# Kernel tuning notes

Hardware: AMD Instinct MI355X
Metric: run time of the kernel (lower is better)

## Reference

```python
import jax, jax.numpy as jnp
import numpy as np

B, K, D, LS, NL = 32, 64, 256, 128, 2


def _xavier(key, shape):
    # torch xavier_uniform for Linear weight [out, in]
    fan_out, fan_in = shape[-2], shape[-1]
    lim = float(np.sqrt(6.0 / (fan_in + fan_out)))
    return jax.random.uniform(key, shape, jnp.float32, -lim, lim)


def setup_inputs():
    key = jax.random.key(0)
    ks = jax.random.split(key, 32)
    inp = {
        "X": jax.random.normal(ks[0], (B, K, D), jnp.float32),
        # per-layer stacked params [NL, ...]
        "k_w": _xavier(ks[1], (NL, D, D)),
        "q_w": _xavier(ks[2], (NL, D, D)),
        "rv_w1": _xavier(ks[3], (NL, D, 2 * D)),
        "rv_b1": jnp.zeros((NL, D), jnp.float32),
        "rv_w2": _xavier(ks[4], (NL, D, D)),
        "rv_b2": jnp.zeros((NL, D), jnp.float32),
        "ln_g": jnp.ones((NL, D), jnp.float32),
        "ln_b": jnp.zeros((NL, D), jnp.float32),
        "mlp_w1": _xavier(ks[5], (NL, D, D)),
        "mlp_b1": jnp.zeros((NL, D), jnp.float32),
        "mlp_w2": _xavier(ks[6], (NL, D, D)),
        "mlp_b2": jnp.zeros((NL, D), jnp.float32),
        "proj_w": _xavier(ks[7], (LS, D)),
        "proj_b": jnp.zeros((LS,), jnp.float32),
        "mu_w": _xavier(ks[8], (LS, LS)),
        "mu_b": jnp.zeros((LS,), jnp.float32),
        "sp_w": _xavier(ks[9], (LS, LS)),
        "sp_b": jnp.zeros((LS,), jnp.float32),
    }
    return inp


def _gelu(x):
    return jax.nn.gelu(x, approximate=False)


def _layernorm(x, g, b, eps=1e-5):
    m = jnp.mean(x, axis=-1, keepdims=True)
    v = jnp.mean((x - m) ** 2, axis=-1, keepdims=True)
    return (x - m) / jnp.sqrt(v + eps) * g + b


def _block(x, kw, qw, rw1, rb1, rw2, rb2, lg, lb, mw1, mb1, mw2, mb2):
    scale = D ** (-0.5)
    x_orig = x
    # pairwise difference r[b,i,j,:] = x[b,i]-x[b,j]
    r = x[:, :, None, :] - x[:, None, :, :]                      # [B,K,K,D]
    xi = jnp.broadcast_to(x[:, :, None, :], (B, K, K, D))
    cat = jnp.concatenate([xi, r], axis=-1)                      # [B,K,K,2D]
    v = _gelu(jnp.einsum('bijc,dc->bijd', cat, rw1) + rb1)
    v = jnp.einsum('bijd,ed->bije', v, rw2) + rb2                # [B,K,K,D]
    k = jnp.einsum('bid,ed->bie', x, kw)
    q = jnp.einsum('bid,ed->bie', x, qw) * scale
    attn = jax.nn.softmax(jnp.einsum('bid,bjd->bij', q, k), axis=2)
    agg = jnp.einsum('bij,bijd->bid', attn, v)
    h = _layernorm(x_orig + agg, lg, lb)
    h = jnp.einsum('bid,ed->bie', _gelu(jnp.einsum('bid,ed->bie', h, mw1) + mb1), mw2) + mb2
    return x_orig + h


def reference(X, k_w, q_w, rv_w1, rv_b1, rv_w2, rv_b2, ln_g, ln_b,
              mlp_w1, mlp_b1, mlp_w2, mlp_b2, proj_w, proj_b,
              mu_w, mu_b, sp_w, sp_b):
    x = X
    for i in range(NL):
        x = _block(x, k_w[i], q_w[i], rv_w1[i], rv_b1[i], rv_w2[i], rv_b2[i],
                   ln_g[i], ln_b[i], mlp_w1[i], mlp_b1[i], mlp_w2[i], mlp_b2[i])
    s = jnp.sum(x, axis=1)                                        # [B,D]
    h = _gelu(s @ proj_w.T + proj_b)                              # [B,LS]
    mu = h @ mu_w.T + mu_b
    scale = jax.nn.softplus(h @ sp_w.T + sp_b)
    return (mu, scale)
```

## Files before the change

### kernel.cpp

```cpp
#include <hip/hip_runtime.h>
#include <hip/hip_bf16.h>


using bf16 = __hip_bfloat16;
typedef short bf16x8 __attribute__((ext_vector_type(8)));
typedef float f32x4 __attribute__((ext_vector_type(4)));

__device__ __forceinline__ float bfu(unsigned short u) { return __uint_as_float(((unsigned)u) << 16); }

__device__ __forceinline__ unsigned short bfr(float v) {
  unsigned u = __float_as_uint(v);
  u += 0x7FFFu + ((u >> 16) & 1u);
  return (unsigned short)(u >> 16);
}

__device__ __forceinline__ float gelu_e(float x) {
  return 0.5f * x * (1.0f + erff(x * 0.7071067811865475f));
}

__device__ __forceinline__ float load_f(const void* p, int i, int fl) {
  if (fl) return bfu(((const unsigned short*)p)[i]);
  return ((const float*)p)[i];
}

__device__ __forceinline__ int block_detect(const void* X) {
  __shared__ int bad_s;
  if (threadIdx.x == 0) bad_s = 0;
  __syncthreads();
  if (threadIdx.x < 256) {
    const float v = bfu(((const unsigned short*)X)[threadIdx.x]);
    if (!(fabsf(v) < 1e6f)) atomicOr(&bad_s, 1);
  }
  __syncthreads();
  return bad_s ? 0 : 1;
}

__device__ __forceinline__ void stage_split4(unsigned short (&aF)[2][4096], int row, int d0, float4 v) {
  ushort4 h, lo;
  h.x = bfr(v.x); h.y = bfr(v.y); h.z = bfr(v.z); h.w = bfr(v.w);
  lo.x = bfr(v.x - bfu(h.x)); lo.y = bfr(v.y - bfu(h.y));
  lo.z = bfr(v.z - bfu(h.z)); lo.w = bfr(v.w - bfu(h.w));
  const int kt = d0 >> 5, lane = row | (((d0 >> 3) & 3) << 4), j = d0 & 7;
  *(ushort4*)&aF[0][kt*512 + lane*8 + j] = h;
  *(ushort4*)&aF[1][kt*512 + lane*8 + j] = lo;
}

__global__ __launch_bounds__(256) void prep_kernel(
    const void* __restrict__ X, const void* __restrict__ kw, const void* __restrict__ qw,
    const void* __restrict__ rw1, const void* __restrict__ rw2, const void* __restrict__ mw1,
    const void* __restrict__ mw2, const void* __restrict__ pw, const void* __restrict__ muw,
    const void* __restrict__ spw,
    const void* __restrict__ rb1, const void* __restrict__ rb2, const void* __restrict__ lng,
    const void* __restrict__ lnb, const void* __restrict__ mb1, const void* __restrict__ mb2,
    const void* __restrict__ pb, const void* __restrict__ mub, const void* __restrict__ spb,
    unsigned short* __restrict__ wfb, unsigned short* __restrict__ w3b,
    float* __restrict__ wh, float* __restrict__ bc)
{
  __shared__ __align__(16) char psm[65536];
  const int fl = block_detect(X);
  const int t = threadIdx.x;
  int blk = blockIdx.x;

  if (blk < 16) {
    unsigned short* ls = (unsigned short*)psm;
    unsigned* lsu = (unsigned*)psm;
    const int l = blk >> 3, kt = blk & 7;
    if (fl) {
      #pragma unroll
      for (int s = 0; s < 4; ++s) {
        const unsigned* sp = (const unsigned*)((s == 0) ? kw : (s == 1) ? qw : rw1);
        const int rstr = (s < 2) ? 128 : 256;
        const int coff = ((s == 3) ? 128 : 0) + kt*16;
        for (int i = t; i < 4096; i += 256) {
          const int e = i >> 4, d2 = i & 15;
          lsu[s*4096 + i] = sp[(l*256 + e)*rstr + coff + d2];
        }
      }
    } else {
      #pragma unroll
      for (int s = 0; s < 4; ++s) {
        const float* sp = (const float*)((s == 0) ? kw : (s == 1) ? qw : rw1);
        const int rstr = (s < 2) ? 256 : 512;
        const int coff = ((s == 3) ? 256 : 0) + kt*32;
        for (int i = t; i < 4096; i += 256) {
          const int e = i >> 4, d2 = i & 15;
          const float f0 = sp[(l*256 + e)*rstr + coff + d2*2];
          const float f1 = sp[(l*256 + e)*rstr + coff + d2*2 + 1];
          lsu[s*4096 + i] = (unsigned)bfr(f0) | ((unsigned)bfr(f1) << 16);
        }
      }
    }
    __syncthreads();
    unsigned* outp = (unsigned*)wfb + (l*8 + kt)*16384;
    for (int f2 = t; f2 < 16384; f2 += 256) {
      const int j2 = f2 & 3, lane = (f2 >> 2) & 63, ntg = f2 >> 8;
      const int seg = ntg >> 4;
      const int e = (ntg & 15)*16 + (lane & 15);
      const int dl = ((lane >> 4) & 3)*8 + j2*2;
      unsigned short r0 = ls[seg*8192 + e*32 + dl];
      unsigned short r1 = ls[seg*8192 + e*32 + dl + 1];
      if (seg == 1) { r0 = bfr(bfu(r0)*0.0625f); r1 = bfr(bfu(r1)*0.0625f); }
      else if (seg == 2) {
        const unsigned short w0 = ls[3*8192 + e*32 + dl];
        const unsigned short w1 = ls[3*8192 + e*32 + dl + 1];
        r0 = bfr(bfu(r0) + bfu(w0)); r1 = bfr(bfu(r1) + bfu(w1));
      }
      outp[f2] = (unsigned)r0 | ((unsigned)r1 << 16);
    }
    return;
  }
  blk -= 16;
  if (blk < 48) {
    unsigned short* ls = (unsigned short*)psm;
    unsigned* lsu = (unsigned*)psm;
    const int l3 = blk >> 3, kt = blk & 7;
    const int l = l3 / 3, gm = l3 % 3;
    const void* src = (gm == 0) ? rw2 : (gm == 1) ? mw1 : mw2;
    if (fl) {
      const unsigned* sp = (const unsigned*)src;
      for (int i = t; i < 4096; i += 256) {
        const int e = i >> 4, d2 = i & 15;
        lsu[i] = sp[(l*256 + e)*128 + kt*16 + d2];
      }
    } else {
      const float* sp = (const float*)src;
      for (int i = t; i < 4096; i += 256) {
        const int e = i >> 4, d2 = i & 15;
        const float f0 = sp[(l*256 + e)*256 + kt*32 + d2*2];
        const float f1 = sp[(l*256 + e)*256 + kt*32 + d2*2 + 1];
        lsu[i] = (unsigned)bfr(f0) | ((unsigned)bfr(f1) << 16);
      }
    }
    __syncthreads();
    unsigned* outp = (unsigned*)w3b + (l3*8 + kt)*4096;
    for (int f2 = t; f2 < 4096; f2 += 256) {
      const int j2 = f2 & 3, lane = (f2 >> 2) & 63, nt = f2 >> 8;
      const int e = nt*16 + (lane & 15);
      const int dl = ((lane >> 4) & 3)*8 + j2*2;
      outp[f2] = (unsigned)ls[e*32 + dl] | ((unsigned)ls[e*32 + dl + 1] << 16);
    }
    return;
  }
  blk -= 48;
  if (blk < 24) {
    float* lsf = (float*)psm;
    if (blk < 8) {
      const int l0 = blk*16;
      if (fl) {
        const unsigned* sp = (const unsigned*)pw;
        for (int i = t; i < 2048; i += 256) {
          const int ll = i >> 7, d2 = i & 127;
          const unsigned u = sp[(l0 + ll)*128 + d2];
          lsf[ll*256 + d2*2]     = __uint_as_float(u << 16);
          lsf[ll*256 + d2*2 + 1] = __uint_as_float(u & 0xffff0000u);
        }
      } else {
        const float* sp = (const float*)pw;
        for (int i = t; i < 4096; i += 256) {
          const int ll = i >> 8, d = i & 255;
          lsf[ll*256 + d] = sp[(l0 + ll)*256 + d];
        }
      }
      __syncthreads();
      for (int i = t; i < 4096; i += 256) {
        const int d = i >> 4, ll = i & 15;
        wh[d*128 + l0 + ll] = lsf[ll*256 + d];
      }
    } else {
      const int grp2 = blk - 8;
      const int isSp = grp2 >> 3;
      const int l0 = (grp2 & 7)*16;
      const void* src = isSp ? spw : muw;
      const int off = isSp ? 49152 : 32768;
      if (fl) {
        const unsigned* sp = (const unsigned*)src;
        for (int i = t; i < 1024; i += 256) {
          const int ll = i >> 6, c2 = i & 63;
          const unsigned u = sp[(l0 + ll)*64 + c2];
          lsf[ll*128 + c2*2]     = __uint_as_float(u << 16);
          lsf[ll*128 + c2*2 + 1] = __uint_as_float(u & 0xffff0000u);
        }
      } else {
        const float* sp = (const float*)src;
        for (int i = t; i < 2048; i += 256) {
          const int ll = i >> 7, c = i & 127;
          lsf[ll*128 + c] = sp[(l0 + ll)*128 + c];
        }
      }
      __syncthreads();
      for (int i = t; i < 2048; i += 256) {
        const int c = i >> 4, ll = i & 15;
        wh[off + c*128 + l0 + ll] = lsf[ll*128 + c];
      }
    }
    return;
  }
  for (int i = t; i < 3456; i += 256) {
    const void* src; int off;
    if (i < 512)       { src = rb1; off = i; }
    else if (i < 1024) { src = rb2; off = i - 512; }
    else if (i < 1536) { src = lng; off = i - 1024; }
    else if (i < 2048) { src = lnb; off = i - 1536; }
    else if (i < 2560) { src = mb1; off = i - 2048; }
    else if (i < 3072) { src = mb2; off = i - 2560; }
    else if (i < 3200) { src = pb;  off = i - 3072; }
    else if (i < 3328) { src = mub; off = i - 3200; }
    else               { src = spb; off = i - 3328; }
    bc[i] = load_f(src, off, fl);
  }
}

template<bool SPLIT, int NTG, int NRR>
__device__ __forceinline__ void k1_body(
    const unsigned short (&aF)[2][4096],
    const unsigned short* __restrict__ wfb, const float* __restrict__ bc,
    float* __restrict__ kq, float* __restrict__ Pf, unsigned* __restrict__ Qpk,
    int l, int row0, int ntg0, int t)
{
  const int w = t >> 6, l64 = t & 63;
  const int col = l64 & 15, quad = l64 >> 4;
  f32x4 acc[NTG];
  #pragma unroll
  for (int i = 0; i < NTG; ++i) acc[i] = (f32x4){0.f, 0.f, 0.f, 0.f};
  for (int kt = 0; kt < 8; ++kt) {
    const bf16x8 ah = *(const bf16x8*)&aF[0][kt*512 + l64*8];
    bf16x8 al;
    if (SPLIT) al = *(const bf16x8*)&aF[1][kt*512 + l64*8];
    #pragma unroll
    for (int i = 0; i < NTG; ++i) {
      const int ntg = ntg0 + w*NTG + i;
      const bf16x8 b = *(const bf16x8*)&wfb[((l*8 + kt)*64 + ntg)*512 + l64*8];
      acc[i] = __builtin_amdgcn_mfma_f32_16x16x32_bf16(ah, b, acc[i], 0, 0, 0);
      if (SPLIT) acc[i] = __builtin_amdgcn_mfma_f32_16x16x32_bf16(al, b, acc[i], 0, 0, 0);
    }
  }
  #pragma unroll
  for (int i = 0; i < NTG; ++i) {
    const int ntg = ntg0 + w*NTG + i;
    if (ntg < 32) {
      const int n = ntg*16 + col;
      #pragma unroll
      for (int r = 0; r < 4; ++r)
        if (NRR == 16 || quad*4 + r < NRR)
          kq[(size_t)(row0 + quad*4 + r)*512 + n] = acc[i][r];
    } else if (ntg < 48) {
      const int c = (ntg - 32)*16 + col;
      const float bias = bc[l*256 + c];
      #pragma unroll
      for (int r = 0; r < 4; ++r)
        if (NRR == 16 || quad*4 + r < NRR)
          Pf[(size_t)(row0 + quad*4 + r)*256 + c] = acc[i][r] + bias;
    } else {
      #pragma unroll
      for (int r = 0; r < 4; ++r) {
        const float v = acc[i][r];
        const float pv = __shfl_xor(v, 1, 64);
        if (!(col & 1) && (NRR == 16 || quad*4 + r < NRR)) {
          const unsigned uu = (unsigned)bfr(v) | ((unsigned)bfr(pv) << 16);
          Qpk[(size_t)(row0 + quad*4 + r)*128 + (ntg - 48)*8 + (col >> 1)] = uu;
        }
      }
    }
  }
}

__global__ __launch_bounds__(256) void k1l0(
    const void* __restrict__ X, const unsigned short* __restrict__ wfb,
    const float* __restrict__ bc, float* __restrict__ kq, float* __restrict__ Pf,
    unsigned* __restrict__ Qpk)
{
  const int fl = block_detect(X);
  __shared__ __align__(16) unsigned short aF[2][4096];
  const int t = threadIdx.x;
  const int mb = (int)blockIdx.x >> 2, nb4 = (int)blockIdx.x & 3;
  const int row0 = mb * 16, ntg0 = nb4 * 16;
  if (fl) {
    for (int i = t; i < 512; i += 256) {
      const int row = i >> 5, d0 = (i & 31) * 8;
      const uint4 u = *(const uint4*)((const unsigned*)X + (size_t)(row0 + row)*128 + (i & 31)*4);
      const int kt = d0 >> 5, lane = row | (((d0 >> 3) & 3) << 4);
      *(uint4*)&aF[0][kt*512 + lane*8] = u;
    }
  } else {
    for (int i = t; i < 1024; i += 256) {
      const int row = i >> 6, d0 = (i & 63) * 4;
      stage_split4(aF, row, d0, *(const float4*)((const float*)X + (size_t)(row0 + row)*256 + d0));
    }
  }
  __syncthreads();
  if (fl) k1_body<false, 4, 16>(aF, wfb, bc, kq, Pf, Qpk, 0, row0, ntg0, t);
  else    k1_body<true,  4, 16>(aF, wfb, bc, kq, Pf, Qpk, 0, row0, ntg0, t);
}

template<int NR>
__device__ __forceinline__ void attn_phase(
    const float* __restrict__ kq, const float* __restrict__ Pf,
    const unsigned* __restrict__ Qpk,
    int row0, int t, float* qg, float* scp, float* als,
    unsigned* Kst, unsigned* Qst)
{
  const int base = row0 & ~63;
  for (int i = t; i < NR*64; i += 512) {
    const int il = i >> 6, d0 = (i & 63)*4;
    *(float4*)&qg[il*256 + d0] = *(const float4*)&kq[(size_t)(row0 + il)*512 + 256 + d0];
  }
  for (int i = t; i < 4096; i += 512) {
    const int row = i >> 6, c4 = i & 63;
    const float4 v = *(const float4*)&kq[(size_t)(base + row)*512 + c4*4];
    Kst[row*132 + c4*2]     = (unsigned)bfr(v.x) | ((unsigned)bfr(v.y) << 16);
    Kst[row*132 + c4*2 + 1] = (unsigned)bfr(v.z) | ((unsigned)bfr(v.w) << 16);
  }
  for (int i = t; i < 2048; i += 512) {
    const int row = i >> 5, c4 = i & 31;
    *(uint4*)&Qst[row*128 + c4*4] = *(const uint4*)&Qpk[(size_t)(base + row)*128 + c4*4];
  }
  __syncthreads();
  const int w = t >> 6, lane = t & 63;
  {
    const int jl = lane & 15, part = lane >> 4;
    const int j = (w & 3)*16 + jl;
    for (int p = 0; p < NR/4; ++p) {
      const int i0 = (p*2 + (w >> 2))*2;
      const unsigned* kr = &Kst[j*132 + part*32];
      const float* q0p = &qg[i0*256 + part*64];
      const float* q1p = &qg[(i0+1)*256 + part*64];
      float s0 = 0.f, s1 = 0.f;
      #pragma unroll
      for (int d2 = 0; d2 < 32; d2 += 2) {
        const unsigned ka = kr[d2], kb = kr[d2 + 1];
        const float4 q0 = *(const float4*)&q0p[d2*2];
        const float4 q1 = *(const float4*)&q1p[d2*2];
        const float k0 = bfu((unsigned short)ka), k1 = bfu((unsigned short)(ka >> 16));
        const float k2 = bfu((unsigned short)kb), k3 = bfu((unsigned short)(kb >> 16));
        s0 = fmaf(k0, q0.x, s0); s0 = fmaf(k1, q0.y, s0);
        s0 = fmaf(k2, q0.z, s0); s0 = fmaf(k3, q0.w, s0);
        s1 = fmaf(k0, q1.x, s1); s1 = fmaf(k1, q1.y, s1);
        s1 = fmaf(k2, q1.z, s1); s1 = fmaf(k3, q1.w, s1);
      }
      s0 += __shfl_xor(s0, 16, 64); s0 += __shfl_xor(s0, 32, 64);
      s1 += __shfl_xor(s1, 16, 64); s1 += __shfl_xor(s1, 32, 64);
      if (part == 0) { scp[i0*64 + j] = s0; scp[(i0+1)*64 + j] = s1; }
    }
  }
  __syncthreads();
  for (int r = w; r < NR; r += 8) {
    float s = scp[r*64 + lane];
    float m = s;
    #pragma unroll
    for (int off = 32; off; off >>= 1) m = fmaxf(m, __shfl_xor(m, off, 64));
    const float e = __expf(s - m);
    float ss = e;
    #pragma unroll
    for (int off = 32; off; off >>= 1) ss += __shfl_xor(ss, off, 64);
    als[r*64 + lane] = e / ss;
  }
  __syncthreads();
  {
    constexpr int RK = NR/4;
    const int cp = t & 127, rb4 = t >> 7;
    float Px[RK], Py[RK], A0[RK], A1[RK], a0[RK], a1[RK];
    #pragma unroll
    for (int k = 0; k < RK; ++k) {
      const float2 P = *(const float2*)&Pf[(size_t)(row0 + rb4*RK + k)*256 + cp*2];
      Px[k] = P.x; Py[k] = P.y;
      A0[k] = -1.702f * P.x; A1[k] = -1.702f * P.y;
      a0[k] = 0.f; a1[k] = 0.f;
    }
    const unsigned* qp = &Qst[cp];
    #pragma unroll 4
    for (int j = 0; j < 64; ++j) {
      const unsigned u = qp[j*128];
      const float q0 = __uint_as_float(u << 16);
      const float q1 = __uint_as_float(u & 0xffff0000u);
      #pragma unroll
      for (int k = 0; k < RK; ++k) {
        const float wgt = als[(rb4*RK + k)*64 + j];
        const float s0 = __builtin_amdgcn_rcpf(1.f + __expf(fmaf(1.702f, q0, A0[k])));
        const float s1 = __builtin_amdgcn_rcpf(1.f + __expf(fmaf(1.702f, q1, A1[k])));
        a0[k] = fmaf(wgt * (Px[k] - q0), s0, a0[k]);
        a1[k] = fmaf(wgt * (Py[k] - q1), s1, a1[k]);
      }
    }
    #pragma unroll
    for (int k = 0; k < RK; ++k) {
      qg[(rb4*RK + k)*256 + cp*2]     = a0[k];
      qg[(rb4*RK + k)*256 + cp*2 + 1] = a1[k];
    }
  }
  __syncthreads();
}

__device__ __forceinline__ void k4_gemm8(
    f32x4 acc[2], const unsigned short (&aF)[2][4096],
    const unsigned short* __restrict__ wg, int w, int l64)
{
  acc[0] = (f32x4){0.f, 0.f, 0.f, 0.f};
  acc[1] = (f32x4){0.f, 0.f, 0.f, 0.f};
  for (int kt = 0; kt < 8; ++kt) {
    const bf16x8 ah = *(const bf16x8*)&aF[0][kt*512 + l64*8];
    const bf16x8 al = *(const bf16x8*)&aF[1][kt*512 + l64*8];
    #pragma unroll
    for (int nt = 0; nt < 2; ++nt) {
      const bf16x8 b = *(const bf16x8*)&wg[((kt*16 + (w*2 + nt))*64 + l64)*8];
      acc[nt] = __builtin_amdgcn_mfma_f32_16x16x32_bf16(ah, b, acc[nt], 0, 0, 0);
      acc[nt] = __builtin_amdgcn_mfma_f32_16x16x32_bf16(al, b, acc[nt], 0, 0, 0);
    }
  }
}

template<bool ADAPT, bool TAIL, int NR>
__device__ __forceinline__ void k4_core(
    const float* gl, const void* __restrict__ xin, int fl,
    float* __restrict__ xout, const unsigned short* __restrict__ wg,
    const float* __restrict__ bc, int l, int row0, int t, bool writeX,
    unsigned short (&aF)[2][4096], float* bufB, float (&mv)[16][2])
{
  const int w = t >> 6, l64 = t & 63;
  const int col = l64 & 15, quad = l64 >> 4;
  const float* rb2c = bc + 512  + l*256;
  const float* lngc = bc + 1024 + l*256;
  const float* lnbc = bc + 1536 + l*256;
  const float* mb1c = bc + 2048 + l*256;
  const float* mb2c = bc + 2560 + l*256;

  for (int i = t; i < NR*64; i += 512) {
    const int row = i >> 6, d0 = (i & 63) * 4;
    stage_split4(aF, row, d0, *(const float4*)&gl[row*256 + d0]);
  }
  if (ADAPT && fl) {
    for (int c = t; c < NR*128; c += 512) {
      const int row = c >> 7, dp = c & 127;
      const unsigned u = ((const unsigned*)xin)[(size_t)(row0 + row)*128 + dp];
      bufB[row*260 + dp*2]     = __uint_as_float(u << 16);
      bufB[row*260 + dp*2 + 1] = __uint_as_float(u & 0xffff0000u);
    }
  } else {
    for (int c = t; c < NR*64; c += 512) {
      const int row = c >> 6, d0 = (c & 63) * 4;
      *(float4*)&bufB[row*260 + d0] = *(const float4*)((const float*)xin + (size_t)(row0 + row)*256 + d0);
    }
  }
  __syncthreads();
  float xtr[2][4];
  #pragma unroll
  for (int nt = 0; nt < 2; ++nt) {
    const int cn = (w*2 + nt)*16 + col;
    #pragma unroll
    for (int r = 0; r < 4; ++r) xtr[nt][r] = bufB[(quad*4 + r)*260 + cn];
  }
  __syncthreads();

  f32x4 acc[2];
  k4_gemm8(acc, aF, wg, w, l64);
  #pragma unroll
  for (int nt = 0; nt < 2; ++nt) {
    const int cn = (w*2 + nt)*16 + col;
    #pragma unroll
    for (int r = 0; r < 4; ++r)
      bufB[(quad*4 + r)*260 + cn] = acc[nt][r] + rb2c[cn] + xtr[nt][r];
  }
  __syncthreads();
  {
    const int row = t >> 5, part = t & 31;
    if (row < NR) {
      float s = 0.f, s2 = 0.f;
      #pragma unroll
      for (int kk = 0; kk < 8; ++kk) {
        const float v = bufB[row*260 + part + kk*32];
        s += v; s2 = fmaf(v, v, s2);
      }
      #pragma unroll
      for (int off = 16; off; off >>= 1) {
        s  += __shfl_xor(s, off, 32);
        s2 += __shfl_xor(s2, off, 32);
      }
      if (part == 0) {
        const float mu = s * (1.f/256.f);
        mv[row][0] = mu;
        mv[row][1] = rsqrtf(fmaf(-mu, mu, s2 * (1.f/256.f)) + 1e-5f);
      }
    }
  }
  __syncthreads();
  for (int i = t; i < NR*64; i += 512) {
    const int row = i >> 6, d0 = (i & 63) * 4;
    float4 v = *(const float4*)&bufB[row*260 + d0];
    const float m = mv[row][0], iv = mv[row][1];
    v.x = (v.x - m)*iv*lngc[d0]   + lnbc[d0];
    v.y = (v.y - m)*iv*lngc[d0+1] + lnbc[d0+1];
    v.z = (v.z - m)*iv*lngc[d0+2] + lnbc[d0+2];
    v.w = (v.w - m)*iv*lngc[d0+3] + lnbc[d0+3];
    stage_split4(aF, row, d0, v);
  }
  __syncthreads();
  k4_gemm8(acc, aF, wg + 65536, w, l64);
  #pragma unroll
  for (int nt = 0; nt < 2; ++nt) {
    const int cn = (w*2 + nt)*16 + col;
    #pragma unroll
    for (int r = 0; r < 4; ++r)
      if (quad*4 + r < NR)
        bufB[(quad*4 + r)*260 + cn] = gelu_e(acc[nt][r] + mb1c[cn]);
  }
  __syncthreads();
  for (int i = t; i < NR*64; i += 512) {
    const int row = i >> 6, d0 = (i & 63) * 4;
    stage_split4(aF, row, d0, *(const float4*)&bufB[row*260 + d0]);
  }
  __syncthreads();
  k4_gemm8(acc, aF, wg + 2*65536, w, l64);
  if (TAIL) {
    #pragma unroll
    for (int nt = 0; nt < 2; ++nt) {
      const int cn = (w*2 + nt)*16 + col;
      #pragma unroll
      for (int r = 0; r < 4; ++r)
        bufB[(quad*4 + r)*260 + cn] = acc[nt][r] + mb2c[cn] + xtr[nt][r];
    }
    __syncthreads();
    for (int i = t; i < NR*64; i += 512) {
      const int row = i >> 6, d0 = (i & 63) * 4;
      const float4 v = *(const float4*)&bufB[row*260 + d0];
      if (writeX) *(float4*)&xout[(size_t)(row0 + row)*256 + d0] = v;
      stage_split4(aF, row, d0, v);
    }
    __syncthreads();
  } else {
    #pragma unroll
    for (int nt = 0; nt < 2; ++nt) {
      const int cn = (w*2 + nt)*16 + col;
      #pragma unroll
      for (int r = 0; r < 4; ++r)
        if (quad*4 + r < NR)
          xout[(size_t)(row0 + quad*4 + r)*256 + cn] = acc[nt][r] + mb2c[cn] + xtr[nt][r];
    }
  }
}

#define SM_QG    0
#define SM_SCP   8192
#define SM_ALS   10240
#define SM_UNION 12288
#define SM_QST   46080
#define SM_AF    12288
#define SM_BUFB  28672
#define SM_MV    45312
#define SM_TOTAL 78848

__device__ __forceinline__ int swz_row0(int bid) {
  const int xcd = bid & 7, j = bid >> 3;
  const int batch = (j & 3)*8 + xcd;
  const int rsub = j >> 2;
  return batch*64 + rsub*8;
}

__global__ __launch_bounds__(512) void kA_attn_mix_kq(
    const unsigned short* __restrict__ w3b, const unsigned short* __restrict__ wfb,
    const float* __restrict__ bc, const void* __restrict__ X, float* __restrict__ x,
    const float* __restrict__ kq, const float* __restrict__ Pf,
    const unsigned* __restrict__ Qpk,
    float* __restrict__ kq1, float* __restrict__ Pf1, unsigned* __restrict__ Qpk1)
{
  const int fl = block_detect(X);
  __shared__ __align__(16) char sm[SM_TOTAL];
  float* qg  = (float*)(sm + SM_QG);
  float* scp = (float*)(sm + SM_SCP);
  float* als = (float*)(sm + SM_ALS);
  unsigned* Kst = (unsigned*)(sm + SM_UNION);
  unsigned* Qst = (unsigned*)(sm + SM_QST);
  unsigned short (&aF)[2][4096] = *reinterpret_cast<unsigned short (*)[2][4096]>(sm + SM_AF);
  float* bufB = (float*)(sm + SM_BUFB);
  float (&mv)[16][2] = *reinterpret_cast<float (*)[16][2]>(sm + SM_MV);
  const int t = threadIdx.x;
  const int row0 = swz_row0((int)blockIdx.x);
  attn_phase<8>(kq, Pf, Qpk, row0, t, qg, scp, als, Kst, Qst);
  k4_core<true, true, 8>(qg, X, fl, x, w3b, bc, 0, row0, t, true, aF, bufB, mv);
  k1_body<true, 8, 8>(aF, wfb, bc, kq1, Pf1, Qpk1, 1, row0, 0, t);
}

__global__ __launch_bounds__(512) void kB_attn_fin(
    const unsigned short* __restrict__ w3b, const float* __restrict__ bc,
    float* __restrict__ x, const float* __restrict__ kq1,
    const float* __restrict__ Pf1, const unsigned* __restrict__ Qpk1)
{
  __shared__ __align__(16) char sm[SM_TOTAL];
  float* qg  = (float*)(sm + SM_QG);
  float* scp = (float*)(sm + SM_SCP);
  float* als = (float*)(sm + SM_ALS);
  unsigned* Kst = (unsigned*)(sm + SM_UNION);
  unsigned* Qst = (unsigned*)(sm + SM_QST);
  unsigned short (&aF)[2][4096] = *reinterpret_cast<unsigned short (*)[2][4096]>(sm + SM_AF);
  float* bufB = (float*)(sm + SM_BUFB);
  float (&mv)[16][2] = *reinterpret_cast<float (*)[16][2]>(sm + SM_MV);
  const int t = threadIdx.x;
  const int row0 = swz_row0((int)blockIdx.x);
  attn_phase<8>(kq1, Pf1, Qpk1, row0, t, qg, scp, als, Kst, Qst);
  k4_core<false, false, 8>(qg, x, 0, x, w3b + 3*65536, bc, 1, row0, t, true, aF, bufB, mv);
}

__global__ __launch_bounds__(256) void k5_head(
    const float* __restrict__ x, const float* __restrict__ wh,
    const float* __restrict__ bc, const void* __restrict__ X,
    void* __restrict__ out)
{
  const int fl = block_detect(X);
  __shared__ float ss[256];
  __shared__ float hh[128];
  const int b = blockIdx.x, t = threadIdx.x;
  {
    const float* xp = x + (size_t)(b << 6)*256 + t;
    float s0 = 0.f, s1 = 0.f, s2 = 0.f, s3 = 0.f;
    for (int i = 0; i < 64; i += 4) {
      s0 += xp[(size_t)(i    )*256];
      s1 += xp[(size_t)(i + 1)*256];
      s2 += xp[(size_t)(i + 2)*256];
      s3 += xp[(size_t)(i + 3)*256];
    }
    ss[t] = (s0 + s1) + (s2 + s3);
  }
  __syncthreads();
  if (t < 128) {
    float acc = bc[3072 + t];
    const float* projT = wh;
    for (int d = 0; d < 256; ++d) acc = fmaf(ss[d], projT[d*128 + t], acc);
    hh[t] = gelu_e(acc);
  }
  __syncthreads();
  float v; int oidx;
  if (t < 128) {
    float acc = bc[3200 + t];
    const float* muT = wh + 32768;
    for (int c = 0; c < 128; ++c) acc = fmaf(hh[c], muT[c*128 + t], acc);
    v = acc; oidx = b*128 + t;
  } else {
    const int u = t - 128;
    float acc = bc[3328 + u];
    const float* spT = wh + 49152;
    for (int c = 0; c < 128; ++c) acc = fmaf(hh[c], spT[c*128 + u], acc);
    v = (acc > 20.f) ? acc : log1pf(__expf(acc));
    oidx = 4096 + b*128 + u;
  }
  if (fl) ((bf16*)out)[oidx] = __float2bfloat16(v);
  else    ((float*)out)[oidx] = v;
}

extern "C" void kernel_launch(void* const* d_in, const int* in_sizes, int n_in,
                              void* d_out, int out_size, void* d_ws, size_t ws_size,
                              hipStream_t stream)
{
  (void)in_sizes; (void)n_in; (void)out_size; (void)ws_size;
  float* ws    = (float*)d_ws;
  float* x     = ws + 16;
  float* kq    = x + 524288;
  float* Pf    = kq + 1048576;
  unsigned* Qpk = (unsigned*)(Pf + 524288);
  float* g     = (float*)(Qpk + 262144);
  unsigned short* wfb = (unsigned short*)(g + 524288);
  unsigned short* w3b = wfb + 524288;
  float* wh    = (float*)(w3b + 393216);
  float* bc    = wh + 65536;
  float* kq1   = bc + 4096;
  float* Pf1   = kq1 + 1048576;
  unsigned* Qpk1 = (unsigned*)(Pf1 + 524288);

  prep_kernel<<<dim3(89), dim3(256), 0, stream>>>(
      d_in[0], d_in[1], d_in[2], d_in[3], d_in[5], d_in[9], d_in[11],
      d_in[13], d_in[15], d_in[17],
      d_in[4], d_in[6], d_in[7], d_in[8], d_in[10], d_in[12],
      d_in[14], d_in[16], d_in[18],
      wfb, w3b, wh, bc);
  k1l0<<<dim3(512), dim3(256), 0, stream>>>(d_in[0], wfb, bc, kq, Pf, Qpk);
  kA_attn_mix_kq<<<dim3(256), dim3(512), 0, stream>>>(
      w3b, wfb, bc, d_in[0], x, kq, Pf, Qpk, kq1, Pf1, Qpk1);
  kB_attn_fin<<<dim3(256), dim3(512), 0, stream>>>(w3b, bc, x, kq1, Pf1, Qpk1);
  k5_head<<<dim3(32), dim3(256), 0, stream>>>(x, wh, bc, d_in[0], (void*)d_out);
}
```

Measured before the change: 202.1 us.

## Double block size of fused attention kernels to 1024 threads

Launches the two fused attention/MLP kernels with 1024 threads per block instead of 512, and rewrites the attention, MLP GEMM and k-projection phases so each wave owns one 16-column tile and one row. The aim is more parallelism per block, shorter per-thread serial loops and better latency hiding, since the grid has only 256 blocks. In exchange each block gets half the registers per thread and more barrier participants, and the k1 body is split into a 16-wave variant.

```diff
diff --git a/kernel.cpp b/kernel.cpp
--- a/kernel.cpp
+++ b/kernel.cpp
@@ -210,7 +210,7 @@
   }
 }
 
-template<bool SPLIT, int NTG, int NRR>
+template<bool SPLIT, int NTG>
 __device__ __forceinline__ void k1_body(
     const unsigned short (&aF)[2][4096],
     const unsigned short* __restrict__ wfb, const float* __restrict__ bc,
@@ -241,6 +241,58 @@
       const int n = ntg*16 + col;
       #pragma unroll
       for (int r = 0; r < 4; ++r)
+        kq[(size_t)(row0 + quad*4 + r)*512 + n] = acc[i][r];
+    } else if (ntg < 48) {
+      const int c = (ntg - 32)*16 + col;
+      const float bias = bc[l*256 + c];
+      #pragma unroll
+      for (int r = 0; r < 4; ++r)
+        Pf[(size_t)(row0 + quad*4 + r)*256 + c] = acc[i][r] + bias;
+    } else {
+      #pragma unroll
+      for (int r = 0; r < 4; ++r) {
+        const float v = acc[i][r];
+        const float pv = __shfl_xor(v, 1, 64);
+        if (!(col & 1)) {
+          const unsigned uu = (unsigned)bfr(v) | ((unsigned)bfr(pv) << 16);
+          Qpk[(size_t)(row0 + quad*4 + r)*128 + (ntg - 48)*8 + (col >> 1)] = uu;
+        }
+      }
+    }
+  }
+}
+
+template<bool SPLIT, int NRR>
+__device__ __forceinline__ void k1_body16(
+    const unsigned short (&aF)[2][4096],
+    const unsigned short* __restrict__ wfb, const float* __restrict__ bc,
+    float* __restrict__ kq, float* __restrict__ Pf, unsigned* __restrict__ Qpk,
+    int l, int row0, int t)
+{
+  const int w = t >> 6, l64 = t & 63;
+  const int col = l64 & 15, quad = l64 >> 4;
+  f32x4 acc[4];
+  #pragma unroll
+  for (int i = 0; i < 4; ++i) acc[i] = (f32x4){0.f, 0.f, 0.f, 0.f};
+  for (int kt = 0; kt < 8; ++kt) {
+    const bf16x8 ah = *(const bf16x8*)&aF[0][kt*512 + l64*8];
+    bf16x8 al;
+    if (SPLIT) al = *(const bf16x8*)&aF[1][kt*512 + l64*8];
+    #pragma unroll
+    for (int i = 0; i < 4; ++i) {
+      const int ntg = w*4 + i;
+      const bf16x8 b = *(const bf16x8*)&wfb[((l*8 + kt)*64 + ntg)*512 + l64*8];
+      acc[i] = __builtin_amdgcn_mfma_f32_16x16x32_bf16(ah, b, acc[i], 0, 0, 0);
+      if (SPLIT) acc[i] = __builtin_amdgcn_mfma_f32_16x16x32_bf16(al, b, acc[i], 0, 0, 0);
+    }
+  }
+  #pragma unroll
+  for (int i = 0; i < 4; ++i) {
+    const int ntg = w*4 + i;
+    if (ntg < 32) {
+      const int n = ntg*16 + col;
+      #pragma unroll
+      for (int r = 0; r < 4; ++r)
         if (NRR == 16 || quad*4 + r < NRR)
           kq[(size_t)(row0 + quad*4 + r)*512 + n] = acc[i][r];
     } else if (ntg < 48) {
@@ -288,29 +340,29 @@
     }
   }
   __syncthreads();
-  if (fl) k1_body<false, 4, 16>(aF, wfb, bc, kq, Pf, Qpk, 0, row0, ntg0, t);
-  else    k1_body<true,  4, 16>(aF, wfb, bc, kq, Pf, Qpk, 0, row0, ntg0, t);
+  if (fl) k1_body<false, 4>(aF, wfb, bc, kq, Pf, Qpk, 0, row0, ntg0, t);
+  else    k1_body<true,  4>(aF, wfb, bc, kq, Pf, Qpk, 0, row0, ntg0, t);
 }
 
 template<int NR>
-__device__ __forceinline__ void attn_phase(
+__device__ __forceinline__ void attn_phase1k(
     const float* __restrict__ kq, const float* __restrict__ Pf,
     const unsigned* __restrict__ Qpk,
     int row0, int t, float* qg, float* scp, float* als,
     unsigned* Kst, unsigned* Qst)
 {
   const int base = row0 & ~63;
-  for (int i = t; i < NR*64; i += 512) {
+  for (int i = t; i < NR*64; i += 1024) {
     const int il = i >> 6, d0 = (i & 63)*4;
     *(float4*)&qg[il*256 + d0] = *(const float4*)&kq[(size_t)(row0 + il)*512 + 256 + d0];
   }
-  for (int i = t; i < 4096; i += 512) {
+  for (int i = t; i < 4096; i += 1024) {
     const int row = i >> 6, c4 = i & 63;
     const float4 v = *(const float4*)&kq[(size_t)(base + row)*512 + c4*4];
     Kst[row*132 + c4*2]     = (unsigned)bfr(v.x) | ((unsigned)bfr(v.y) << 16);
     Kst[row*132 + c4*2 + 1] = (unsigned)bfr(v.z) | ((unsigned)bfr(v.w) << 16);
   }
-  for (int i = t; i < 2048; i += 512) {
+  for (int i = t; i < 2048; i += 1024) {
     const int row = i >> 5, c4 = i & 31;
     *(uint4*)&Qst[row*128 + c4*4] = *(const uint4*)&Qpk[(size_t)(base + row)*128 + c4*4];
   }
@@ -319,31 +371,30 @@
   {
     const int jl = lane & 15, part = lane >> 4;
     const int j = (w & 3)*16 + jl;
-    for (int p = 0; p < NR/4; ++p) {
-      const int i0 = (p*2 + (w >> 2))*2;
-      const unsigned* kr = &Kst[j*132 + part*32];
-      const float* q0p = &qg[i0*256 + part*64];
-      const float* q1p = &qg[(i0+1)*256 + part*64];
-      float s0 = 0.f, s1 = 0.f;
-      #pragma unroll
-      for (int d2 = 0; d2 < 32; d2 += 2) {
-        const unsigned ka = kr[d2], kb = kr[d2 + 1];
-        const float4 q0 = *(const float4*)&q0p[d2*2];
-        const float4 q1 = *(const float4*)&q1p[d2*2];
-        const float k0 = bfu((unsigned short)ka), k1 = bfu((unsigned short)(ka >> 16));
-        const float k2 = bfu((unsigned short)kb), k3 = bfu((unsigned short)(kb >> 16));
-        s0 = fmaf(k0, q0.x, s0); s0 = fmaf(k1, q0.y, s0);
-        s0 = fmaf(k2, q0.z, s0); s0 = fmaf(k3, q0.w, s0);
-        s1 = fmaf(k0, q1.x, s1); s1 = fmaf(k1, q1.y, s1);
-        s1 = fmaf(k2, q1.z, s1); s1 = fmaf(k3, q1.w, s1);
-      }
-      s0 += __shfl_xor(s0, 16, 64); s0 += __shfl_xor(s0, 32, 64);
-      s1 += __shfl_xor(s1, 16, 64); s1 += __shfl_xor(s1, 32, 64);
-      if (part == 0) { scp[i0*64 + j] = s0; scp[(i0+1)*64 + j] = s1; }
-    }
-  }
-  __syncthreads();
-  for (int r = w; r < NR; r += 8) {
+    const int i0 = (w >> 2) * 2;
+    const unsigned* kr = &Kst[j*132 + part*32];
+    const float* q0p = &qg[i0*256 + part*64];
+    const float* q1p = &qg[(i0+1)*256 + part*64];
+    float s0 = 0.f, s1 = 0.f;
+    #pragma unroll
+    for (int d2 = 0; d2 < 32; d2 += 2) {
+      const unsigned ka = kr[d2], kb = kr[d2 + 1];
+      const float4 q0 = *(const float4*)&q0p[d2*2];
+      const float4 q1 = *(const float4*)&q1p[d2*2];
+      const float k0 = bfu((unsigned short)ka), k1 = bfu((unsigned short)(ka >> 16));
+      const float k2 = bfu((unsigned short)kb), k3 = bfu((unsigned short)(kb >> 16));
+      s0 = fmaf(k0, q0.x, s0); s0 = fmaf(k1, q0.y, s0);
+      s0 = fmaf(k2, q0.z, s0); s0 = fmaf(k3, q0.w, s0);
+      s1 = fmaf(k0, q1.x, s1); s1 = fmaf(k1, q1.y, s1);
+      s1 = fmaf(k2, q1.z, s1); s1 = fmaf(k3, q1.w, s1);
+    }
+    s0 += __shfl_xor(s0, 16, 64); s0 += __shfl_xor(s0, 32, 64);
+    s1 += __shfl_xor(s1, 16, 64); s1 += __shfl_xor(s1, 32, 64);
+    if (part == 0) { scp[i0*64 + j] = s0; scp[(i0+1)*64 + j] = s1; }
+  }
+  __syncthreads();
+  if (w < NR) {
+    const int r = w;
     float s = scp[r*64 + lane];
     float m = s;
     #pragma unroll
@@ -356,60 +407,46 @@
   }
   __syncthreads();
   {
-    constexpr int RK = NR/4;
-    const int cp = t & 127, rb4 = t >> 7;
-    float Px[RK], Py[RK], A0[RK], A1[RK], a0[RK], a1[RK];
-    #pragma unroll
-    for (int k = 0; k < RK; ++k) {
-      const float2 P = *(const float2*)&Pf[(size_t)(row0 + rb4*RK + k)*256 + cp*2];
-      Px[k] = P.x; Py[k] = P.y;
-      A0[k] = -1.702f * P.x; A1[k] = -1.702f * P.y;
-      a0[k] = 0.f; a1[k] = 0.f;
-    }
+    const int cp = t & 127, rb = t >> 7;
+    const float2 P = *(const float2*)&Pf[(size_t)(row0 + rb)*256 + cp*2];
+    const float A0 = -1.702f * P.x, A1 = -1.702f * P.y;
+    float a0 = 0.f, a1 = 0.f;
     const unsigned* qp = &Qst[cp];
+    const float* ap = &als[rb*64];
     #pragma unroll 4
     for (int j = 0; j < 64; ++j) {
       const unsigned u = qp[j*128];
+      const float wgt = ap[j];
       const float q0 = __uint_as_float(u << 16);
       const float q1 = __uint_as_float(u & 0xffff0000u);
-      #pragma unroll
-      for (int k = 0; k < RK; ++k) {
-        const float wgt = als[(rb4*RK + k)*64 + j];
-        const float s0 = __builtin_amdgcn_rcpf(1.f + __expf(fmaf(1.702f, q0, A0[k])));
-        const float s1 = __builtin_amdgcn_rcpf(1.f + __expf(fmaf(1.702f, q1, A1[k])));
-        a0[k] = fmaf(wgt * (Px[k] - q0), s0, a0[k]);
-        a1[k] = fmaf(wgt * (Py[k] - q1), s1, a1[k]);
-      }
-    }
-    #pragma unroll
-    for (int k = 0; k < RK; ++k) {
-      qg[(rb4*RK + k)*256 + cp*2]     = a0[k];
-      qg[(rb4*RK + k)*256 + cp*2 + 1] = a1[k];
-    }
-  }
-  __syncthreads();
-}
-
-__device__ __forceinline__ void k4_gemm8(
-    f32x4 acc[2], const unsigned short (&aF)[2][4096],
+      const float s0 = __builtin_amdgcn_rcpf(1.f + __expf(fmaf(1.702f, q0, A0)));
+      const float s1 = __builtin_amdgcn_rcpf(1.f + __expf(fmaf(1.702f, q1, A1)));
+      a0 = fmaf(wgt * (P.x - q0), s0, a0);
+      a1 = fmaf(wgt * (P.y - q1), s1, a1);
+    }
+    qg[rb*256 + cp*2]     = a0;
+    qg[rb*256 + cp*2 + 1] = a1;
+  }
+  __syncthreads();
+}
+
+__device__ __forceinline__ f32x4 k4_gemm16(
+    const unsigned short (&aF)[2][4096],
     const unsigned short* __restrict__ wg, int w, int l64)
 {
-  acc[0] = (f32x4){0.f, 0.f, 0.f, 0.f};
-  acc[1] = (f32x4){0.f, 0.f, 0.f, 0.f};
+  f32x4 acc = (f32x4){0.f, 0.f, 0.f, 0.f};
   for (int kt = 0; kt < 8; ++kt) {
     const bf16x8 ah = *(const bf16x8*)&aF[0][kt*512 + l64*8];
     const bf16x8 al = *(const bf16x8*)&aF[1][kt*512 + l64*8];
-    #pragma unroll
-    for (int nt = 0; nt < 2; ++nt) {
-      const bf16x8 b = *(const bf16x8*)&wg[((kt*16 + (w*2 + nt))*64 + l64)*8];
-      acc[nt] = __builtin_amdgcn_mfma_f32_16x16x32_bf16(ah, b, acc[nt], 0, 0, 0);
-      acc[nt] = __builtin_amdgcn_mfma_f32_16x16x32_bf16(al, b, acc[nt], 0, 0, 0);
-    }
-  }
+    const bf16x8 b = *(const bf16x8*)&wg[((kt*16 + w)*64 + l64)*8];
+    acc = __builtin_amdgcn_mfma_f32_16x16x32_bf16(ah, b, acc, 0, 0, 0);
+    acc = __builtin_amdgcn_mfma_f32_16x16x32_bf16(al, b, acc, 0, 0, 0);
+  }
+  return acc;
 }
 
 template<bool ADAPT, bool TAIL, int NR>
-__device__ __forceinline__ void k4_core(
+__device__ __forceinline__ void k4_core1k(
     const float* gl, const void* __restrict__ xin, int fl,
     float* __restrict__ xout, const unsigned short* __restrict__ wg,
     const float* __restrict__ bc, int l, int row0, int t, bool writeX,
@@ -417,48 +454,40 @@
 {
   const int w = t >> 6, l64 = t & 63;
   const int col = l64 & 15, quad = l64 >> 4;
+  const int cn = w*16 + col;
   const float* rb2c = bc + 512  + l*256;
   const float* lngc = bc + 1024 + l*256;
   const float* lnbc = bc + 1536 + l*256;
   const float* mb1c = bc + 2048 + l*256;
   const float* mb2c = bc + 2560 + l*256;
 
-  for (int i = t; i < NR*64; i += 512) {
+  for (int i = t; i < NR*64; i += 1024) {
     const int row = i >> 6, d0 = (i & 63) * 4;
     stage_split4(aF, row, d0, *(const float4*)&gl[row*256 + d0]);
   }
   if (ADAPT && fl) {
-    for (int c = t; c < NR*128; c += 512) {
+    for (int c = t; c < NR*128; c += 1024) {
       const int row = c >> 7, dp = c & 127;
       const unsigned u = ((const unsigned*)xin)[(size_t)(row0 + row)*128 + dp];
       bufB[row*260 + dp*2]     = __uint_as_float(u << 16);
       bufB[row*260 + dp*2 + 1] = __uint_as_float(u & 0xffff0000u);
     }
   } else {
-    for (int c = t; c < NR*64; c += 512) {
+    for (int c = t; c < NR*64; c += 1024) {
       const int row = c >> 6, d0 = (c & 63) * 4;
       *(float4*)&bufB[row*260 + d0] = *(const float4*)((const float*)xin + (size_t)(row0 + row)*256 + d0);
     }
   }
   __syncthreads();
-  float xtr[2][4];
+  float xtr[4];
   #pragma unroll
-  for (int nt = 0; nt < 2; ++nt) {
-    const int cn = (w*2 + nt)*16 + col;
-    #pragma unroll
-    for (int r = 0; r < 4; ++r) xtr[nt][r] = bufB[(quad*4 + r)*260 + cn];
-  }
-  __syncthreads();
-
-  f32x4 acc[2];
-  k4_gemm8(acc, aF, wg, w, l64);
+  for (int r = 0; r < 4; ++r) xtr[r] = bufB[(quad*4 + r)*260 + cn];
+  __syncthreads();
+
+  f32x4 acc = k4_gemm16(aF, wg, w, l64);
   #pragma unroll
-  for (int nt = 0; nt < 2; ++nt) {
-    const int cn = (w*2 + nt)*16 + col;
-    #pragma unroll
-    for (int r = 0; r < 4; ++r)
-      bufB[(quad*4 + r)*260 + cn] = acc[nt][r] + rb2c[cn] + xtr[nt][r];
-  }
+  for (int r = 0; r < 4; ++r)
+    bufB[(quad*4 + r)*260 + cn] = acc[r] + rb2c[cn] + xtr[r];
   __syncthreads();
   {
     const int row = t >> 5, part = t & 31;
@@ -482,7 +511,7 @@
     }
   }
   __syncthreads();
-  for (int i = t; i < NR*64; i += 512) {
+  for (int i = t; i < NR*64; i += 1024) {
     const int row = i >> 6, d0 = (i & 63) * 4;
     float4 v = *(const float4*)&bufB[row*260 + d0];
     const float m = mv[row][0], iv = mv[row][1];
@@ -493,32 +522,24 @@
     stage_split4(aF, row, d0, v);
   }
   __syncthreads();
-  k4_gemm8(acc, aF, wg + 65536, w, l64);
+  acc = k4_gemm16(aF, wg + 65536, w, l64);
   #pragma unroll
-  for (int nt = 0; nt < 2; ++nt) {
-    const int cn = (w*2 + nt)*16 + col;
+  for (int r = 0; r < 4; ++r)
+    if (quad*4 + r < NR)
+      bufB[(quad*4 + r)*260 + cn] = gelu_e(acc[r] + mb1c[cn]);
+  __syncthreads();
+  for (int i = t; i < NR*64; i += 1024) {
+    const int row = i >> 6, d0 = (i & 63) * 4;
+    stage_split4(aF, row, d0, *(const float4*)&bufB[row*260 + d0]);
+  }
+  __syncthreads();
+  acc = k4_gemm16(aF, wg + 2*65536, w, l64);
+  if (TAIL) {
     #pragma unroll
     for (int r = 0; r < 4; ++r)
-      if (quad*4 + r < NR)
-        bufB[(quad*4 + r)*260 + cn] = gelu_e(acc[nt][r] + mb1c[cn]);
-  }
-  __syncthreads();
-  for (int i = t; i < NR*64; i += 512) {
-    const int row = i >> 6, d0 = (i & 63) * 4;
-    stage_split4(aF, row, d0, *(const float4*)&bufB[row*260 + d0]);
-  }
-  __syncthreads();
-  k4_gemm8(acc, aF, wg + 2*65536, w, l64);
-  if (TAIL) {
-    #pragma unroll
-    for (int nt = 0; nt < 2; ++nt) {
-      const int cn = (w*2 + nt)*16 + col;
-      #pragma unroll
-      for (int r = 0; r < 4; ++r)
-        bufB[(quad*4 + r)*260 + cn] = acc[nt][r] + mb2c[cn] + xtr[nt][r];
-    }
+      bufB[(quad*4 + r)*260 + cn] = acc[r] + mb2c[cn] + xtr[r];
     __syncthreads();
-    for (int i = t; i < NR*64; i += 512) {
+    for (int i = t; i < NR*64; i += 1024) {
       const int row = i >> 6, d0 = (i & 63) * 4;
       const float4 v = *(const float4*)&bufB[row*260 + d0];
       if (writeX) *(float4*)&xout[(size_t)(row0 + row)*256 + d0] = v;
@@ -527,13 +548,9 @@
     __syncthreads();
   } else {
     #pragma unroll
-    for (int nt = 0; nt < 2; ++nt) {
-      const int cn = (w*2 + nt)*16 + col;
-      #pragma unroll
-      for (int r = 0; r < 4; ++r)
-        if (quad*4 + r < NR)
-          xout[(size_t)(row0 + quad*4 + r)*256 + cn] = acc[nt][r] + mb2c[cn] + xtr[nt][r];
-    }
+    for (int r = 0; r < 4; ++r)
+      if (quad*4 + r < NR)
+        xout[(size_t)(row0 + quad*4 + r)*256 + cn] = acc[r] + mb2c[cn] + xtr[r];
   }
 }
 
@@ -554,7 +571,7 @@
   return batch*64 + rsub*8;
 }
 
-__global__ __launch_bounds__(512) void kA_attn_mix_kq(
+__global__ __launch_bounds__(1024) void kA_attn_mix_kq(
     const unsigned short* __restrict__ w3b, const unsigned short* __restrict__ wfb,
     const float* __restrict__ bc, const void* __restrict__ X, float* __restrict__ x,
     const float* __restrict__ kq, const float* __restrict__ Pf,
@@ -573,12 +590,12 @@
   float (&mv)[16][2] = *reinterpret_cast<float (*)[16][2]>(sm + SM_MV);
   const int t = threadIdx.x;
   const int row0 = swz_row0((int)blockIdx.x);
-  attn_phase<8>(kq, Pf, Qpk, row0, t, qg, scp, als, Kst, Qst);
-  k4_core<true, true, 8>(qg, X, fl, x, w3b, bc, 0, row0, t, true, aF, bufB, mv);
-  k1_body<true, 8, 8>(aF, wfb, bc, kq1, Pf1, Qpk1, 1, row0, 0, t);
-}
-
-__global__ __launch_bounds__(512) void kB_attn_fin(
+  attn_phase1k<8>(kq, Pf, Qpk, row0, t, qg, scp, als, Kst, Qst);
+  k4_core1k<true, true, 8>(qg, X, fl, x, w3b, bc, 0, row0, t, true, aF, bufB, mv);
+  k1_body16<true, 8>(aF, wfb, bc, kq1, Pf1, Qpk1, 1, row0, t);
+}
+
+__global__ __launch_bounds__(1024) void kB_attn_fin(
     const unsigned short* __restrict__ w3b, const float* __restrict__ bc,
     float* __restrict__ x, const float* __restrict__ kq1,
     const float* __restrict__ Pf1, const unsigned* __restrict__ Qpk1)
@@ -594,8 +611,8 @@
   float (&mv)[16][2] = *reinterpret_cast<float (*)[16][2]>(sm + SM_MV);
   const int t = threadIdx.x;
   const int row0 = swz_row0((int)blockIdx.x);
-  attn_phase<8>(kq1, Pf1, Qpk1, row0, t, qg, scp, als, Kst, Qst);
-  k4_core<false, false, 8>(qg, x, 0, x, w3b + 3*65536, bc, 1, row0, t, true, aF, bufB, mv);
+  attn_phase1k<8>(kq1, Pf1, Qpk1, row0, t, qg, scp, als, Kst, Qst);
+  k4_core1k<false, false, 8>(qg, x, 0, x, w3b + 3*65536, bc, 1, row0, t, true, aF, bufB, mv);
 }
 
 __global__ __launch_bounds__(256) void k5_head(
@@ -670,8 +687,8 @@
       d_in[14], d_in[16], d_in[18],
       wfb, w3b, wh, bc);
   k1l0<<<dim3(512), dim3(256), 0, stream>>>(d_in[0], wfb, bc, kq, Pf, Qpk);
-  kA_attn_mix_kq<<<dim3(256), dim3(512), 0, stream>>>(
+  kA_attn_mix_kq<<<dim3(256), dim3(1024), 0, stream>>>(
       w3b, wfb, bc, d_in[0], x, kq, Pf, Qpk, kq1, Pf1, Qpk1);
-  kB_attn_fin<<<dim3(256), dim3(512), 0, stream>>>(w3b, bc, x, kq1, Pf1, Qpk1);
+  kB_attn_fin<<<dim3(256), dim3(1024), 0, stream>>>(w3b, bc, x, kq1, Pf1, Qpk1);
   k5_head<<<dim3(32), dim3(256), 0, stream>>>(x, wh, bc, d_in[0], (void*)d_out);
 }
```

Measured after the change: 187.2 us (median of 2 runs). 1.08x faster.
